# Kernel optimization log

Hardware: AMD Instinct MI355X
Metric: run time of the kernel (lower is better)

## Reference

```python
import jax, jax.numpy as jnp
import numpy as np

TOTAL_INSTANCES = 131072
NUM_BAGS = 64
FEATURE_DIM = 512
HIDDEN_DIM = 256


def setup_inputs() -> dict:
    key = jax.random.key(0)
    k1, k2, k3 = jax.random.split(key, 3)
    instance_features = jax.random.normal(k1, (TOTAL_INSTANCES, FEATURE_DIM), dtype=jnp.float32)
    # Equal-sized bags (sum(bag_sizes) == TOTAL_INSTANCES); the reference handles ragged sizes too.
    bag_sizes = jnp.full((NUM_BAGS,), TOTAL_INSTANCES // NUM_BAGS, dtype=jnp.int32)
    W1 = jax.random.normal(k2, (FEATURE_DIM, HIDDEN_DIM), dtype=jnp.float32) * (1.0 / np.sqrt(FEATURE_DIM))
    b1 = jnp.zeros((HIDDEN_DIM,), dtype=jnp.float32)
    W2 = jax.random.normal(k3, (HIDDEN_DIM, 1), dtype=jnp.float32) * (1.0 / np.sqrt(HIDDEN_DIM))
    b2 = jnp.zeros((1,), dtype=jnp.float32)
    return {
        "instance_features": instance_features,
        "bag_sizes": bag_sizes,
        "W1": W1,
        "b1": b1,
        "W2": W2,
        "b2": b2,
    }


def reference(instance_features, bag_sizes, W1, b1, W2, b2):
    # Attention MLP: Linear -> Tanh -> Linear  => scores [T, 1]
    scores = jnp.tanh(instance_features @ W1 + b1) @ W2 + b2
    # Faithful to the original: softmax over dim=0 GLOBALLY across all instances.
    weights = jax.nn.softmax(scores, axis=0)  # [T, 1]
    T = instance_features.shape[0]
    B = bag_sizes.shape[0]
    # Ragged bag membership: instance i belongs to the first bag whose cumulative
    # size exceeds i.
    offsets = jnp.cumsum(bag_sizes)  # [B]
    seg_ids = jnp.searchsorted(offsets, jnp.arange(T), side="right")  # [T]
    # Per-bag weighted sum of instances: [B, feature_dim]
    return jax.ops.segment_sum(instance_features * weights, seg_ids, num_segments=B)
```

## Files before the change

### kernel.cpp

```cpp
#include <hip/hip_runtime.h>

typedef __attribute__((ext_vector_type(8))) short short8;
typedef __attribute__((ext_vector_type(4))) float floatx4;

#define FDIM 512
#define HDIM 256

__device__ __forceinline__ unsigned short f2bf(float f) {
  unsigned int u = __float_as_uint(f);
  u += 0x7fffu + ((u >> 16) & 1u);
  return (unsigned short)(u >> 16);
}

__device__ __forceinline__ short8 pack2(floatx4 a, floatx4 b) {
  short8 r;
  r[0] = (short)f2bf(a[0]); r[1] = (short)f2bf(a[1]);
  r[2] = (short)f2bf(a[2]); r[3] = (short)f2bf(a[3]);
  r[4] = (short)f2bf(b[0]); r[5] = (short)f2bf(b[1]);
  r[6] = (short)f2bf(b[2]); r[7] = (short)f2bf(b[3]);
  return r;
}

__device__ __forceinline__ float fast_tanh(float x) {
  x = fminf(15.0f, fmaxf(-15.0f, x));
  float e = __expf(2.0f * x);
  return (e - 1.0f) / (e + 1.0f);
}

#define GLOAD_A(r0, r1, p)                                                     \
  do {                                                                         \
    asm volatile("global_load_dwordx4 %0, %1, off"                             \
                 : "=v"(r0) : "v"(p) : "memory");                              \
    asm volatile("global_load_dwordx4 %0, %1, off offset:16"                   \
                 : "=v"(r1) : "v"(p) : "memory");                              \
  } while (0)

#define GLOAD_B(r, p)                                                          \
  do {                                                                         \
    asm volatile("global_load_dwordx4 %0, %1, off"                             \
                 : "=v"(r[0]) : "v"(p) : "memory");                            \
    asm volatile("global_load_dwordx4 %0, %1, off offset:256"                  \
                 : "=v"(r[1]) : "v"(p) : "memory");                            \
    asm volatile("global_load_dwordx4 %0, %1, off offset:512"                  \
                 : "=v"(r[2]) : "v"(p) : "memory");                            \
    asm volatile("global_load_dwordx4 %0, %1, off offset:768"                  \
                 : "=v"(r[3]) : "v"(p) : "memory");                            \
  } while (0)

__global__ void __launch_bounds__(256)
k0_pack_w1(const float* __restrict__ W1, unsigned short* __restrict__ W1B,
           float* __restrict__ out) {
  int tid = threadIdx.x;
  int idx = blockIdx.x * 256 + tid;
  if (blockIdx.x < 128) out[blockIdx.x * 256 + tid] = 0.0f;
  int k = idx >> 8;
  int n = idx & 255;
  int s = k >> 5, r = k & 31, oct = r >> 3, e = r & 7;
  W1B[s * 8192 + oct * 2048 + n * 8 + e] = f2bf(W1[idx]);
}

__global__ void __launch_bounds__(256, 2)
k1_fused(const float* __restrict__ X,
         const unsigned short* __restrict__ W1B,
         const float* __restrict__ b1,
         const float* __restrict__ W2,
         const int* __restrict__ bag_sizes,
         int nbags,
         float* __restrict__ out,
         float* __restrict__ partials) {
  __shared__ __align__(16) unsigned char smem[66816];
  unsigned short* As = (unsigned short*)smem;
  float* scpart = (float*)(smem + 65536);
  float* es_s   = (float*)(smem + 66560);

  const int tid  = threadIdx.x;
  const int wn   = tid >> 6;
  const int lane = tid & 63;
  const int l15  = lane & 15;
  const int l4   = lane >> 4;
  const long row0 = (long)blockIdx.x * 64;

  floatx4 acc[4][4];
  #pragma unroll
  for (int m = 0; m < 4; m++)
    #pragma unroll
    for (int n = 0; n < 4; n++)
      acc[m][n] = (floatx4){0.f, 0.f, 0.f, 0.f};

  const int arow = tid >> 2;
  const int aoct = tid & 3;
  const float* xsrc = X + (row0 + arow) * FDIM + aoct * 8;
  const unsigned short* bsrc = W1B + l4 * 2048 + (wn * 64 + l15) * 8;

  floatx4 va0, va1, vb0, vb1;
  short8 br0[4], br1[4], br2[4];

  GLOAD_A(va0, va1, xsrc);
  GLOAD_B(br0, bsrc);
  GLOAD_A(vb0, vb1, xsrc + 32);
  GLOAD_B(br1, bsrc + 8192);

  #pragma unroll
  for (int t = 0; t < 16; ++t) {
    if (t < 15) asm volatile("s_waitcnt vmcnt(10)" ::: "memory");
    else        asm volatile("s_waitcnt vmcnt(4)" ::: "memory");
    __builtin_amdgcn_sched_barrier(0);
    {
      short8 a = ((t & 1) == 0) ? pack2(va0, va1) : pack2(vb0, vb1);
      int slot = t * 4 + aoct;
      *(short8*)(As + (slot * 64 + (arow ^ (slot & 7))) * 8) = a;
    }
    asm volatile("s_waitcnt lgkmcnt(0)" ::: "memory");
    __builtin_amdgcn_sched_barrier(0);
    __builtin_amdgcn_s_barrier();
    if (t < 14) {
      const float* pp = xsrc + (t + 2) * 32;
      if ((t & 1) == 0) GLOAD_A(va0, va1, pp);
      else              GLOAD_A(vb0, vb1, pp);
      const unsigned short* bp = bsrc + (t + 2) * 8192;
      if (((t + 2) % 3) == 0)      GLOAD_B(br0, bp);
      else if (((t + 2) % 3) == 1) GLOAD_B(br1, bp);
      else                         GLOAD_B(br2, bp);
    }
    if (t < 14)       asm volatile("s_waitcnt vmcnt(12)" ::: "memory");
    else if (t == 14) asm volatile("s_waitcnt vmcnt(6)" ::: "memory");
    else              asm volatile("s_waitcnt vmcnt(0)" ::: "memory");
    __builtin_amdgcn_sched_barrier(0);
    const int slotc = t * 4 + l4;
    const int gg = slotc & 7;
    short8 af[4];
    #pragma unroll
    for (int m = 0; m < 4; ++m)
      af[m] = *(const short8*)(As + (slotc * 64 + ((m * 16 + l15) ^ gg)) * 8);
    const short8* bcur = ((t % 3) == 0) ? br0 : ((t % 3) == 1) ? br1 : br2;
    #pragma unroll
    for (int n = 0; n < 4; ++n)
      #pragma unroll
      for (int m = 0; m < 4; ++m)
        acc[m][n] = __builtin_amdgcn_mfma_f32_16x16x32_bf16(af[m], bcur[n], acc[m][n], 0, 0, 0);
  }

  float rowacc[16];
  #pragma unroll
  for (int i = 0; i < 16; i++) rowacc[i] = 0.f;
  #pragma unroll
  for (int n = 0; n < 4; n++) {
    int c = wn * 64 + n * 16 + l15;
    float b1c = b1[c];
    float w2c = W2[c];
    #pragma unroll
    for (int m = 0; m < 4; m++)
      #pragma unroll
      for (int j = 0; j < 4; j++) {
        float h = fast_tanh(acc[m][n][j] + b1c);
        rowacc[m * 4 + j] = fmaf(h, w2c, rowacc[m * 4 + j]);
      }
  }
  #pragma unroll
  for (int i = 0; i < 16; i++) {
    float v = rowacc[i];
    v += __shfl_xor(v, 1, 64);
    v += __shfl_xor(v, 2, 64);
    v += __shfl_xor(v, 4, 64);
    v += __shfl_xor(v, 8, 64);
    rowacc[i] = v;
  }
  if (l15 == 0) {
    #pragma unroll
    for (int m = 0; m < 4; m++)
      #pragma unroll
      for (int j = 0; j < 4; j++)
        scpart[wn * 64 + m * 16 + l4 * 4 + j] = rowacc[m * 4 + j];
  }
  __syncthreads();

  if (tid < 64) {
    float sv = scpart[0 * 64 + tid] + scpart[1 * 64 + tid] +
               scpart[2 * 64 + tid] + scpart[3 * 64 + tid];
    float ev = __expf(sv);
    es_s[tid] = ev;
    float v = ev;
    v += __shfl_xor(v, 1, 64);
    v += __shfl_xor(v, 2, 64);
    v += __shfl_xor(v, 4, 64);
    v += __shfl_xor(v, 8, 64);
    v += __shfl_xor(v, 16, 64);
    v += __shfl_xor(v, 32, 64);
    if (tid == 0) partials[blockIdx.x] = v;
  }
  __syncthreads();

  const int s  = tid >> 2;
  const int p  = tid & 3;
  const int gp = s & 7;
  const int fbase = (s >> 2) * 32 + (s & 3) * 8;
  const unsigned short* abase = As + s * 512;

  int bag = 0; long cum = 0;
  while (bag + 1 < nbags && cum + (long)bag_sizes[bag] <= row0) {
    cum += bag_sizes[bag]; ++bag;
  }
  long bagEnd = cum + (long)bag_sizes[bag];

  int rs = 0;
  while (rs < 64) {
    int se = (int)(bagEnd - row0 < 64 ? bagEnd - row0 : 64);
    float pa[8];
    #pragma unroll
    for (int e = 0; e < 8; ++e) pa[e] = 0.f;
    #pragma unroll
    for (int j = 0; j < 16; ++j) {
      int r = p + 4 * j;
      if (r >= rs && r < se) {
        float w = es_s[r];
        short8 xv = *(const short8*)(abase + ((r ^ gp) * 8));
        const unsigned int* ui = (const unsigned int*)&xv;
        #pragma unroll
        for (int d = 0; d < 4; ++d) {
          float xlo = __uint_as_float(ui[d] << 16);
          float xhi = __uint_as_float(ui[d] & 0xffff0000u);
          pa[2 * d]     = fmaf(xlo, w, pa[2 * d]);
          pa[2 * d + 1] = fmaf(xhi, w, pa[2 * d + 1]);
        }
      }
    }
    #pragma unroll
    for (int e = 0; e < 8; ++e) {
      pa[e] += __shfl_xor(pa[e], 1, 64);
      pa[e] += __shfl_xor(pa[e], 2, 64);
    }
    if (p == 0 && se > rs) {
      float* op = out + (long)bag * FDIM + fbase;
      #pragma unroll
      for (int e = 0; e < 8; ++e) atomicAdd(op + e, pa[e]);
    }
    rs = se;
    if (rs < 64) {
      ++bag;
      if (bag >= nbags) { bagEnd = row0 + 64; bag = nbags - 1; }
      else bagEnd += (long)bag_sizes[bag];
    }
  }
}

__global__ void __launch_bounds__(256)
k2_scale(const float* __restrict__ partials, int nparts, float* __restrict__ out) {
  __shared__ float wred[4];
  int tid = threadIdx.x;
  float sL = 0.f;
  for (int j = tid; j < nparts; j += 256) sL += partials[j];
  #pragma unroll
  for (int m = 1; m < 64; m <<= 1) sL += __shfl_xor(sL, m, 64);
  if ((tid & 63) == 0) wred[tid >> 6] = sL;
  __syncthreads();
  float invZ = 1.0f / (wred[0] + wred[1] + wred[2] + wred[3]);
  int i = blockIdx.x * 256 + tid;
  out[i] = out[i] * invZ;
}

extern "C" void kernel_launch(void* const* d_in, const int* in_sizes, int n_in,
                              void* d_out, int out_size, void* d_ws, size_t ws_size,
                              hipStream_t stream) {
  const float* X         = (const float*)d_in[0];
  const int*   bag_sizes = (const int*)d_in[1];
  const float* W1        = (const float*)d_in[2];
  const float* b1        = (const float*)d_in[3];
  const float* W2        = (const float*)d_in[4];
  float* out = (float*)d_out;

  const int T     = in_sizes[0] / FDIM;
  const int nbags = in_sizes[1];
  const int nblk  = T / 64;

  char* ws = (char*)d_ws;
  unsigned short* W1B = (unsigned short*)ws;
  float* partials = (float*)(ws + 262144);

  hipLaunchKernelGGL(k0_pack_w1, dim3(512), dim3(256), 0, stream, W1, W1B, out);
  hipLaunchKernelGGL(k1_fused, dim3(nblk), dim3(256), 0, stream,
                     X, W1B, b1, W2, bag_sizes, nbags, out, partials);
  hipLaunchKernelGGL(k2_scale, dim3((nbags * FDIM) / 256), dim3(256), 0, stream,
                     partials, nblk, out);
}
```

Baseline: 124.6 us.

## Shrink LDS to double-buffered A tiles and re-read X for weighted bag sum

```diff
diff --git a/kernel.cpp b/kernel.cpp
--- a/kernel.cpp
+++ b/kernel.cpp
@@ -68,10 +68,9 @@
          int nbags,
          float* __restrict__ out,
          float* __restrict__ partials) {
-  __shared__ __align__(16) unsigned char smem[66816];
-  unsigned short* As = (unsigned short*)smem;
-  float* scpart = (float*)(smem + 65536);
-  float* es_s   = (float*)(smem + 66560);
+  __shared__ __align__(16) unsigned short As[2][2048];
+  __shared__ float scpart[256];
+  __shared__ float es_s[64];
 
   const int tid  = threadIdx.x;
   const int wn   = tid >> 6;
@@ -93,46 +92,43 @@
   const unsigned short* bsrc = W1B + l4 * 2048 + (wn * 64 + l15) * 8;
 
   floatx4 va0, va1, vb0, vb1;
-  short8 br0[4], br1[4], br2[4];
+  short8 br0[4], br1[4];
 
   GLOAD_A(va0, va1, xsrc);
   GLOAD_B(br0, bsrc);
   GLOAD_A(vb0, vb1, xsrc + 32);
-  GLOAD_B(br1, bsrc + 8192);
 
   #pragma unroll
   for (int t = 0; t < 16; ++t) {
-    if (t < 15) asm volatile("s_waitcnt vmcnt(10)" ::: "memory");
+    if (t < 15) asm volatile("s_waitcnt vmcnt(6)" ::: "memory");
     else        asm volatile("s_waitcnt vmcnt(4)" ::: "memory");
     __builtin_amdgcn_sched_barrier(0);
     {
       short8 a = ((t & 1) == 0) ? pack2(va0, va1) : pack2(vb0, vb1);
-      int slot = t * 4 + aoct;
-      *(short8*)(As + (slot * 64 + (arow ^ (slot & 7))) * 8) = a;
+      *(short8*)(&As[t & 1][arow * 32 + aoct * 8]) = a;
     }
     asm volatile("s_waitcnt lgkmcnt(0)" ::: "memory");
     __builtin_amdgcn_sched_barrier(0);
     __builtin_amdgcn_s_barrier();
+    if (t < 15) {
+      const unsigned short* bp = bsrc + (t + 1) * 8192;
+      if (((t + 1) & 1) == 0) GLOAD_B(br0, bp);
+      else                    GLOAD_B(br1, bp);
+    }
     if (t < 14) {
       const float* pp = xsrc + (t + 2) * 32;
       if ((t & 1) == 0) GLOAD_A(va0, va1, pp);
       else              GLOAD_A(vb0, vb1, pp);
-      const unsigned short* bp = bsrc + (t + 2) * 8192;
-      if (((t + 2) % 3) == 0)      GLOAD_B(br0, bp);
-      else if (((t + 2) % 3) == 1) GLOAD_B(br1, bp);
-      else                         GLOAD_B(br2, bp);
-    }
-    if (t < 14)       asm volatile("s_waitcnt vmcnt(12)" ::: "memory");
+    }
+    if (t < 14)       asm volatile("s_waitcnt vmcnt(8)" ::: "memory");
     else if (t == 14) asm volatile("s_waitcnt vmcnt(6)" ::: "memory");
     else              asm volatile("s_waitcnt vmcnt(0)" ::: "memory");
     __builtin_amdgcn_sched_barrier(0);
-    const int slotc = t * 4 + l4;
-    const int gg = slotc & 7;
     short8 af[4];
     #pragma unroll
     for (int m = 0; m < 4; ++m)
-      af[m] = *(const short8*)(As + (slotc * 64 + ((m * 16 + l15) ^ gg)) * 8);
-    const short8* bcur = ((t % 3) == 0) ? br0 : ((t % 3) == 1) ? br1 : br2;
+      af[m] = *(const short8*)(&As[t & 1][(m * 16 + l15) * 32 + l4 * 8]);
+    const short8* bcur = ((t & 1) == 0) ? br0 : br1;
     #pragma unroll
     for (int n = 0; n < 4; ++n)
       #pragma unroll
@@ -190,11 +186,9 @@
   }
   __syncthreads();
 
-  const int s  = tid >> 2;
-  const int p  = tid & 3;
-  const int gp = s & 7;
-  const int fbase = (s >> 2) * 32 + (s & 3) * 8;
-  const unsigned short* abase = As + s * 512;
+  float4* red4 = (float4*)As;
+  const int f = (tid & 127) * 4;
+  const int r = tid >> 7;
 
   int bag = 0; long cum = 0;
   while (bag + 1 < nbags && cum + (long)bag_sizes[bag] <= row0) {
@@ -205,35 +199,23 @@
   int rs = 0;
   while (rs < 64) {
     int se = (int)(bagEnd - row0 < 64 ? bagEnd - row0 : 64);
-    float pa[8];
-    #pragma unroll
-    for (int e = 0; e < 8; ++e) pa[e] = 0.f;
-    #pragma unroll
-    for (int j = 0; j < 16; ++j) {
-      int r = p + 4 * j;
-      if (r >= rs && r < se) {
-        float w = es_s[r];
-        short8 xv = *(const short8*)(abase + ((r ^ gp) * 8));
-        const unsigned int* ui = (const unsigned int*)&xv;
-        #pragma unroll
-        for (int d = 0; d < 4; ++d) {
-          float xlo = __uint_as_float(ui[d] << 16);
-          float xhi = __uint_as_float(ui[d] & 0xffff0000u);
-          pa[2 * d]     = fmaf(xlo, w, pa[2 * d]);
-          pa[2 * d + 1] = fmaf(xhi, w, pa[2 * d + 1]);
-        }
-      }
-    }
-    #pragma unroll
-    for (int e = 0; e < 8; ++e) {
-      pa[e] += __shfl_xor(pa[e], 1, 64);
-      pa[e] += __shfl_xor(pa[e], 2, 64);
-    }
-    if (p == 0 && se > rs) {
-      float* op = out + (long)bag * FDIM + fbase;
-      #pragma unroll
-      for (int e = 0; e < 8; ++e) atomicAdd(op + e, pa[e]);
-    }
+    if (se < rs) se = rs;
+    float ax = 0.f, ay = 0.f, az = 0.f, aw = 0.f;
+    for (int i = rs + r; i < se; i += 2) {
+      float w = es_s[i];
+      float4 x = *(const float4*)(X + (row0 + i) * FDIM + f);
+      ax = fmaf(x.x, w, ax); ay = fmaf(x.y, w, ay);
+      az = fmaf(x.z, w, az); aw = fmaf(x.w, w, aw);
+    }
+    if (r == 1) red4[tid & 127] = (float4){ax, ay, az, aw};
+    __syncthreads();
+    if (r == 0 && se > rs) {
+      float4 o = red4[tid];
+      float* op = out + (long)bag * FDIM + f;
+      atomicAdd(op + 0, ax + o.x); atomicAdd(op + 1, ay + o.y);
+      atomicAdd(op + 2, az + o.z); atomicAdd(op + 3, aw + o.w);
+    }
+    __syncthreads();
     rs = se;
     if (rs < 64) {
       ++bag;
```

Measured after the change: 121.9 us. 1.02x faster.
